# Optimization experiments

Measured on AMD Instinct MI355X. Metric: run time of the kernel, lower is better.

## Reference

```python
import jax, jax.numpy as jnp
import numpy as np

D_LOW = 32
LAGS = [1, 2, 4, 8]
# Upper-triangular pair indices (offset=1), matching torch.triu_indices(d_low, d_low, 1)
IDX_I, IDX_J = np.triu_indices(D_LOW, k=1)
IDX_I = jnp.asarray(IDX_I)
IDX_J = jnp.asarray(IDX_J)
EPS = 1e-6


def setup_inputs() -> dict:
    key = jax.random.key(0)
    ks = jax.random.split(key, 7)
    b, n, d_model = 4, 4096, 1024
    d_plucker = D_LOW * (D_LOW - 1) // 2  # 496
    s = lambda fan_in: 1.0 / np.sqrt(fan_in)
    return {
        "x": jax.random.normal(ks[0], (b, n, d_model), dtype=jnp.float32),
        "W_red": jax.random.normal(ks[1], (d_model, D_LOW), dtype=jnp.float32) * s(d_model),
        "b_red": jax.random.normal(ks[2], (D_LOW,), dtype=jnp.float32) * s(d_model),
        "W_exp": jax.random.normal(ks[3], (d_plucker, d_model), dtype=jnp.float32) * s(d_plucker),
        "b_exp": jax.random.normal(ks[4], (d_model,), dtype=jnp.float32) * s(d_plucker),
        "W_gate": jax.random.normal(ks[5], (2 * d_model, d_model), dtype=jnp.float32) * s(2 * d_model),
        "b_gate": jax.random.normal(ks[6], (d_model,), dtype=jnp.float32) * s(2 * d_model),
    }


def reference(x, W_red, b_red, W_exp, b_exp, W_gate, b_gate):
    b, n, _ = x.shape
    d_plucker = D_LOW * (D_LOW - 1) // 2
    z = x @ W_red + b_red  # [b, n, d_low]
    plucker_total = jnp.zeros((b, n, d_plucker), dtype=x.dtype)
    counts = jnp.zeros((b, n, 1), dtype=x.dtype)
    for lag in LAGS:
        if lag <= 0 or lag >= n:
            continue
        z_curr = z[:, lag:, :]   # [b, n-lag, d_low]
        z_past = z[:, :-lag, :]  # [b, n-lag, d_low]
        # Antisymmetric Plucker coordinates over upper-triangular index pairs
        p = (z_curr[:, :, IDX_I] * z_past[:, :, IDX_J]
             - z_curr[:, :, IDX_J] * z_past[:, :, IDX_I])  # [b, n-lag, d_plucker]
        norm = jnp.linalg.norm(p, axis=-1, keepdims=True)
        p = p / jnp.maximum(norm, EPS)
        plucker_total = plucker_total.at[:, lag:, :].add(p)
        counts = counts.at[:, lag:, :].add(1.0)
    counts = jnp.maximum(counts, 1.0)
    plucker_avg = plucker_total / counts
    g_avg = plucker_avg @ W_exp + b_exp  # [b, n, d_model]
    concat = jnp.concatenate([x, g_avg], axis=-1)  # [b, n, 2*d_model]
    gate = jax.nn.sigmoid(concat @ W_gate + b_gate)
    return gate * x + (1.0 - gate) * g_avg
```

## Files before the change

### kernel.cpp

```cpp
#include <hip/hip_runtime.h>
#include <hip/hip_bf16.h>
#include <math.h>

#define B_DIM   4
#define N_DIM   4096
#define D_MODEL 1024
#define D_LOW   32
#define NPAIR   496
#define NROWS   (B_DIM * N_DIM)
#define KPAD3   512
#define LDA2    1536

typedef __bf16 bf16;
typedef __bf16 bf16x8 __attribute__((ext_vector_type(8)));
typedef __bf16 bf16x4 __attribute__((ext_vector_type(4)));
typedef float  f32x4  __attribute__((ext_vector_type(4)));

#define GLOAD_LDS16(g, l) __builtin_amdgcn_global_load_lds( \
    (__attribute__((address_space(1))) void*)(g),           \
    (__attribute__((address_space(3))) void*)(l), 16, 0, 0)

__global__ __launch_bounds__(256) void prep_misc(const float* __restrict__ Wr,
                                                 bf16* __restrict__ WrT,
                                                 const float* __restrict__ We,
                                                 const float* __restrict__ be,
                                                 bf16* __restrict__ WeB) {
    __shared__ float tile[32][33];
    const int bx = blockIdx.x;
    const int t  = threadIdx.x;
    if (bx < 32) {
        const int kb = bx * 32;
        {
            int k = t >> 3, c4 = (t & 7) * 4;
            float4 v = *reinterpret_cast<const float4*>(&Wr[(size_t)(kb + k) * 32 + c4]);
            tile[k][c4 + 0] = v.x; tile[k][c4 + 1] = v.y;
            tile[k][c4 + 2] = v.z; tile[k][c4 + 3] = v.w;
        }
        __syncthreads();
        {
            int c = t >> 3, kq = (t & 7) * 4;
            bf16x4 o = { (bf16)tile[kq + 0][c], (bf16)tile[kq + 1][c],
                         (bf16)tile[kq + 2][c], (bf16)tile[kq + 3][c] };
            *reinterpret_cast<bf16x4*>(&WrT[(size_t)c * 1024 + kb + kq]) = o;
        }
    } else {
        size_t o = ((size_t)(bx - 32) * 256 + t) * 4;
        int row = (int)(o >> 10), col = (int)(o & 1023);
        float4 v = {0.f, 0.f, 0.f, 0.f};
        if (row < NPAIR)       v = *reinterpret_cast<const float4*>(&We[(size_t)row * 1024 + col]);
        else if (row == NPAIR) v = *reinterpret_cast<const float4*>(&be[col]);
        bf16x4 b = { (bf16)v.x, (bf16)v.y, (bf16)v.z, (bf16)v.w };
        *reinterpret_cast<bf16x4*>(&WeB[o]) = b;
    }
}

__global__ __launch_bounds__(256) void k1_mfma(const float* __restrict__ x,
                                               const bf16* __restrict__ WrT,
                                               bf16* __restrict__ a2,
                                               float* __restrict__ zpart) {
    const int t    = threadIdx.x;
    const int wv   = t >> 6, lane = t & 63;
    const int l15  = lane & 15, lhi = lane >> 4;
    const int kc   = blockIdx.x;
    const int mt   = blockIdx.y;
    const int row  = mt * 64 + wv * 16 + l15;
    const int kb   = kc * 256;

    f32x4 accz[2] = { (f32x4){0.f,0.f,0.f,0.f}, (f32x4){0.f,0.f,0.f,0.f} };

#pragma unroll
    for (int ks = 0; ks < 8; ++ks) {
        const int k0 = kb + ks * 32 + lhi * 8;
        const float4 u0 = *reinterpret_cast<const float4*>(&x[(size_t)row * 1024 + k0]);
        const float4 u1 = *reinterpret_cast<const float4*>(&x[(size_t)row * 1024 + k0 + 4]);
        bf16x8 af = { (bf16)u0.x, (bf16)u0.y, (bf16)u0.z, (bf16)u0.w,
                      (bf16)u1.x, (bf16)u1.y, (bf16)u1.z, (bf16)u1.w };
        *reinterpret_cast<bf16x8*>(&a2[(size_t)row * LDA2 + k0]) = af;
        const bf16x8 b0 = *reinterpret_cast<const bf16x8*>(
            &WrT[(size_t)l15 * 1024 + kb + ks * 32 + lhi * 8]);
        const bf16x8 b1 = *reinterpret_cast<const bf16x8*>(
            &WrT[(size_t)(16 + l15) * 1024 + kb + ks * 32 + lhi * 8]);
        accz[0] = __builtin_amdgcn_mfma_f32_16x16x32_bf16(af, b0, accz[0], 0, 0, 0);
        accz[1] = __builtin_amdgcn_mfma_f32_16x16x32_bf16(af, b1, accz[1], 0, 0, 0);
    }
#pragma unroll
    for (int cg = 0; cg < 2; ++cg)
#pragma unroll
        for (int r = 0; r < 4; ++r) {
            const int rout = mt * 64 + wv * 16 + lhi * 4 + r;
            zpart[((size_t)kc * NROWS + rout) * 32 + cg * 16 + l15] = accz[cg][r];
        }
}

__global__ __launch_bounds__(256) void k2_plucker(const float* __restrict__ zpart,
                                                  const float* __restrict__ br,
                                                  bf16* __restrict__ a2) {
    const int wv   = threadIdx.x >> 6;
    const int lane = threadIdx.x & 63;
    const int row  = blockIdx.x * 4 + wv;
    const int t    = row & (N_DIM - 1);
    const int c    = lane & 31;
    const float bias = br[c];

    float zc = bias;
#pragma unroll
    for (int p = 0; p < 4; ++p)
        zc += zpart[((size_t)p * NROWS + row) * 32 + c];

    float zp[4];
    float red[9];
    red[0] = zc * zc;
#pragma unroll
    for (int li = 0; li < 4; ++li) {
        const int lag = 1 << li;
        float v = 0.f;
        if (t >= lag) {
            v = bias;
#pragma unroll
            for (int p = 0; p < 4; ++p)
                v += zpart[((size_t)p * NROWS + (row - lag)) * 32 + c];
        }
        zp[li] = v;
        red[1 + li] = zc * zp[li];
        red[5 + li] = zp[li] * zp[li];
    }
#pragma unroll
    for (int m = 1; m < 32; m <<= 1) {
#pragma unroll
        for (int i = 0; i < 9; ++i) red[i] += __shfl_xor(red[i], m);
    }
    float cnt = 0.f;
#pragma unroll
    for (int li = 0; li < 4; ++li) cnt += (t >= (1 << li)) ? 1.f : 0.f;
    const float inv = 1.f / fmaxf(cnt, 1.f);

    float w = 0.f;
#pragma unroll
    for (int li = 0; li < 4; ++li) {
        float n2 = fmaxf(red[0] * red[5 + li] - red[1 + li] * red[1 + li], 0.f);
        float nr = sqrtf(n2);
        float s  = (t >= (1 << li)) ? inv / fmaxf(nr, 1e-6f) : 0.f;
        w += s * zp[li];
    }

#pragma unroll
    for (int u = 0; u < 8; ++u) {
        const int k = u * 64 + lane;
        float v = 0.f;
        if (k < NPAIR) {
            int kk = k, i = 0;
            while (kk >= 31 - i) { kk -= 31 - i; ++i; }
            const int j = i + 1 + kk;
            float zci = __shfl(zc, i), zcj = __shfl(zc, j);
            float wi  = __shfl(w, i),  wj  = __shfl(w, j);
            v = zci * wj - zcj * wi;
        }
        a2[(size_t)row * LDA2 + 1024 + k] = (bf16)v;
    }
}

__global__ __launch_bounds__(256) void transpose2(const float* __restrict__ Wg,
                                                  const float* __restrict__ We,
                                                  bf16* __restrict__ BcT,
                                                  bf16* __restrict__ WgbT,
                                                  bf16* __restrict__ WeT) {
    __shared__ float tile[32][36];
    const int z = blockIdx.z;
    const float* src = (z == 0) ? Wg : (z == 1) ? (Wg + (size_t)1024 * 1024) : We;
    bf16* dst  = (z == 0) ? BcT : (z == 1) ? WgbT : WeT;
    const int Kpad = (z == 0) ? 1536 : (z == 1) ? 1024 : 512;
    const int Ksrc = (z == 2) ? NPAIR : 1024;
    const int kb = blockIdx.x * 32;
    if (kb >= Kpad) return;
    const int nb = blockIdx.y * 32;
    const int t  = threadIdx.x;
    int li = t * 4;
    int kl = li >> 5, nl = li & 31;
    float4 v = {0.f, 0.f, 0.f, 0.f};
    if (kb + kl < Ksrc)
        v = *reinterpret_cast<const float4*>(&src[(size_t)(kb + kl) * 1024 + nb + nl]);
    tile[kl][nl + 0] = v.x; tile[kl][nl + 1] = v.y;
    tile[kl][nl + 2] = v.z; tile[kl][nl + 3] = v.w;
    __syncthreads();
    int nl2 = li >> 5, kl2 = li & 31;
    bf16x4 o = { (bf16)tile[kl2 + 0][nl2], (bf16)tile[kl2 + 1][nl2],
                 (bf16)tile[kl2 + 2][nl2], (bf16)tile[kl2 + 3][nl2] };
    *reinterpret_cast<bf16x4*>(&dst[(size_t)(nb + nl2) * Kpad + kb + kl2]) = o;
}

__global__ __launch_bounds__(256) void wcomb_wave(const bf16* __restrict__ WgbT,
                                                  const bf16* __restrict__ WeB,
                                                  bf16* __restrict__ BcT) {
    const int t    = threadIdx.x;
    const int wv   = t >> 6, lane = t & 63;
    const int l15  = lane & 15, lhi = lane >> 4;
    const int kk0  = blockIdx.x * 16;
    const int n0   = blockIdx.y * 64 + wv * 16;
    f32x4 acc = (f32x4){0.f, 0.f, 0.f, 0.f};
#pragma unroll 8
    for (int kb = 0; kb < 1024; kb += 32) {
        const bf16x8 af = *reinterpret_cast<const bf16x8*>(
            &WgbT[(size_t)(n0 + l15) * 1024 + kb + lhi * 8]);
        const bf16x8 bf = *reinterpret_cast<const bf16x8*>(
            &WeB[(size_t)(kk0 + l15) * 1024 + kb + lhi * 8]);
        acc = __builtin_amdgcn_mfma_f32_16x16x32_bf16(af, bf, acc, 0, 0, 0);
    }
#pragma unroll
    for (int r = 0; r < 4; ++r) {
        const int n = n0 + lhi * 4 + r;
        BcT[(size_t)n * 1536 + 1024 + kk0 + l15] = (bf16)acc[r];
    }
}

template <int KDIM, int LDAp, int LDBp, bool GATE>
__global__ __launch_bounds__(512, 2) void gemmoc(const bf16* __restrict__ A,
                                                 const bf16* __restrict__ Bt,
                                                 const float* __restrict__ bias,
                                                 const bf16* __restrict__ gsrc,
                                                 bf16* __restrict__ gdst,
                                                 float* __restrict__ out) {
    extern __shared__ char lds[];
    const int t    = threadIdx.x;
    const int w    = t >> 6, lane = t & 63;
    const int wr   = w >> 2, wc = w & 3;
    const int l15  = lane & 15, lhi = lane >> 4;

    const int fid = blockIdx.x;
    const int xcd = fid & 7, loc = fid >> 3;
    const int mb  = (xcd * 8 + (loc >> 2)) * 256;
    const int nb  = (loc & 3) * 256;

    const int srow = t >> 2;
    const int scol = ((t & 3) ^ (srow & 3)) * 8;
    const size_t aOff = (size_t)(mb + srow) * LDAp + scol;
    const size_t bOff = (size_t)(nb + srow) * LDBp + scol;
    char* const ldsA = lds;
    char* const ldsB = lds + 32768;

#define STAGE_A(d, h, kb) \
    GLOAD_LDS16(A + aOff + (size_t)((h) * 128) * LDAp + (kb), \
                ldsA + (d) * 16384 + (h) * 8192 + t * 16)
#define STAGE_B(d, h, kb) \
    GLOAD_LDS16(Bt + bOff + (size_t)((h) * 128) * LDBp + (kb), \
                ldsB + (d) * 16384 + (h) * 8192 + t * 16)

    const int swx = (l15 & 3) << 4;
#define LDAF(d, mq_) do { const char* Ab_ = ldsA + (d) * 16384 + wr * 8192; \
    _Pragma("unroll") for (int mf = 0; mf < 4; ++mf) { \
        int lin = ((mq_) * 64 + mf * 16 + l15) * 64 + ((lhi * 16) ^ swx); \
        afr[mf] = *reinterpret_cast<const bf16x8*>(Ab_ + lin); } } while (0)
#define LDBF(dst, d, nq_) do { const char* Bb_ = ldsB + (d) * 16384 + (wc >> 1) * 8192; \
    _Pragma("unroll") for (int nf = 0; nf < 2; ++nf) { \
        int lin = ((wc & 1) * 64 + (nq_) * 32 + nf * 16 + l15) * 64 + ((lhi * 16) ^ swx); \
        dst[nf] = *reinterpret_cast<const bf16x8*>(Bb_ + lin); } } while (0)
#define MMA(bset, mq_, nq_) do { __builtin_amdgcn_s_setprio(1); \
    _Pragma("unroll") for (int mf = 0; mf < 4; ++mf) \
    _Pragma("unroll") for (int nf = 0; nf < 2; ++nf) \
        acc[(mq_) * 4 + mf][(nq_) * 2 + nf] = __builtin_amdgcn_mfma_f32_16x16x32_bf16( \
            afr[mf], bset[nf], acc[(mq_) * 4 + mf][(nq_) * 2 + nf], 0, 0, 0); \
    __builtin_amdgcn_s_setprio(0); } while (0)
#define BAR() asm volatile("s_barrier" ::: "memory")

    f32x4 acc[8][4];
#pragma unroll
    for (int i = 0; i < 8; ++i)
#pragma unroll
        for (int j = 0; j < 4; ++j) acc[i][j] = (f32x4){0.f, 0.f, 0.f, 0.f};
    bf16x8 afr[4], bfr0[2], bfrB[2];

    STAGE_A(0, 0, 0);  STAGE_A(0, 1, 0);  STAGE_B(0, 0, 0);  STAGE_B(0, 1, 0);
    STAGE_A(1, 0, 32); STAGE_A(1, 1, 32); STAGE_B(1, 0, 32); STAGE_B(1, 1, 32);

    const int NT    = KDIM / 32;
    const int ITERS = NT / 2;
    for (int it = 0; it < ITERS; ++it) {
        const int kA = (it * 2 + 2) * 32;
        const int kB = (it * 2 + 3) * 32;
        const bool p2 = (it * 2 + 2) < NT;
        const bool p3 = (it * 2 + 3) < NT;

        asm volatile("s_waitcnt vmcnt(4)" ::: "memory");
        BAR();
        LDAF(0, 0); LDBF(bfr0, 0, 0);
        MMA(bfr0, 0, 0);
        BAR();
        LDBF(bfrB, 0, 1);
        MMA(bfrB, 0, 1);
        BAR();
        if (p2) { STAGE_B(0, 0, kA); STAGE_B(0, 1, kA); }
        LDAF(0, 1);
        MMA(bfrB, 1, 1);
        BAR();
        if (p2) { STAGE_A(0, 0, kA); STAGE_A(0, 1, kA); }
        MMA(bfr0, 1, 0);

        if (p2) asm volatile("s_waitcnt vmcnt(4)" ::: "memory");
        else    asm volatile("s_waitcnt vmcnt(0)" ::: "memory");
        BAR();
        LDAF(1, 0); LDBF(bfr0, 1, 0);
        MMA(bfr0, 0, 0);
        BAR();
        LDBF(bfrB, 1, 1);
        MMA(bfrB, 0, 1);
        BAR();
        if (p3) { STAGE_B(1, 0, kB); STAGE_B(1, 1, kB); }
        LDAF(1, 1);
        MMA(bfrB, 1, 1);
        BAR();
        if (p3) { STAGE_A(1, 0, kB); STAGE_A(1, 1, kB); }
        MMA(bfr0, 1, 0);
    }
#undef STAGE_A
#undef STAGE_B
#undef LDAF
#undef LDBF
#undef MMA
#undef BAR

#pragma unroll
    for (int mi = 0; mi < 8; ++mi) {
#pragma unroll
        for (int nf = 0; nf < 4; ++nf) {
            const int col = nb + wc * 64 + nf * 16 + l15;
            float bv = bias[col];
            if constexpr (GATE)
                bv += (float)Bt[(size_t)col * LDBp + 1024 + NPAIR];
#pragma unroll
            for (int r = 0; r < 4; ++r) {
                const int row = mb + wr * 128 + mi * 16 + lhi * 4 + r;
                float v = acc[mi][nf][r] + bv;
                if constexpr (GATE) {
                    float gate = 1.f / (1.f + expf(-v));
                    float xv = (float)A[(size_t)row * LDAp + col];
                    float gv = (float)gsrc[(size_t)row * D_MODEL + col];
                    out[(size_t)row * D_MODEL + col] = gate * xv + (1.f - gate) * gv;
                } else {
                    gdst[(size_t)row * D_MODEL + col] = (bf16)v;
                }
            }
        }
    }
}

extern "C" void kernel_launch(void* const* d_in, const int* in_sizes, int n_in,
                              void* d_out, int out_size, void* d_ws, size_t ws_size,
                              hipStream_t stream) {
    const float* x  = (const float*)d_in[0];
    const float* Wr = (const float*)d_in[1];
    const float* br = (const float*)d_in[2];
    const float* We = (const float*)d_in[3];
    const float* be = (const float*)d_in[4];
    const float* Wg = (const float*)d_in[5];
    const float* bg = (const float*)d_in[6];
    float* out = (float*)d_out;

    char* ws = (char*)d_ws;
    bf16*  gbuf  = (bf16*)(ws);
    float* zpart = (float*)(ws);
    bf16*  A2    = (bf16*)(ws + (32u << 20));
    bf16*  WeT   = (bf16*)(ws + (80u << 20));
    bf16*  BcT   = (bf16*)(ws + (81u << 20));
    bf16*  WgbT  = (bf16*)(ws + (84u << 20));
    bf16*  WeB   = (bf16*)(ws + (86u << 20));
    bf16*  WrT   = (bf16*)(ws + (88u << 20));

    (void)hipFuncSetAttribute(reinterpret_cast<const void*>(&gemmoc<KPAD3, LDA2, KPAD3, false>),
                              hipFuncAttributeMaxDynamicSharedMemorySize, 65536);
    (void)hipFuncSetAttribute(reinterpret_cast<const void*>(&gemmoc<1536, LDA2, 1536, true>),
                              hipFuncAttributeMaxDynamicSharedMemorySize, 65536);

    prep_misc<<<544, 256, 0, stream>>>(Wr, WrT, We, be, WeB);
    transpose2<<<dim3(32, 32, 3), 256, 0, stream>>>(Wg, We, BcT, WgbT, WeT);
    wcomb_wave<<<dim3(32, 16), 256, 0, stream>>>(WgbT, WeB, BcT);
    k1_mfma<<<dim3(4, 256), 256, 0, stream>>>(x, WrT, A2, zpart);
    k2_plucker<<<NROWS / 4, 256, 0, stream>>>(zpart, br, A2);

    gemmoc<KPAD3, LDA2, KPAD3, false><<<256, 512, 65536, stream>>>(
        A2 + 1024, WeT, be, nullptr, gbuf, nullptr);
    gemmoc<1536, LDA2, 1536, true><<<256, 512, 65536, stream>>>(
        A2, BcT, bg, gbuf, nullptr, out);
}
```

Before: 165.4 us.

## Replace 256x256 eight-wave GEMM with 128x128 four-wave K64 double-buffered GEMM

Both GEMMs switch from 256x256 output tiles on 512-thread blocks, with an interleaved ping-pong schedule, to 128x128 tiles on 256-thread blocks. Each block now stages K=64 slices with an 8-way XOR swizzle and uses a simple double-buffered loop. The grid grows from 256 to 1024 blocks, which should spread work better across CUs and simplify scheduling. The cost is lower reuse per tile, so global and L2 traffic for A and B roughly doubles, and the fine-grained compute/load interleaving is lost.

```diff
diff --git a/kernel.cpp b/kernel.cpp
--- a/kernel.cpp
+++ b/kernel.cpp
@@ -213,7 +213,7 @@
 }
 
 template <int KDIM, int LDAp, int LDBp, bool GATE>
-__global__ __launch_bounds__(512, 2) void gemmoc(const bf16* __restrict__ A,
+__global__ __launch_bounds__(256, 2) void gemm2c(const bf16* __restrict__ A,
                                                  const bf16* __restrict__ Bt,
                                                  const float* __restrict__ bias,
                                                  const bf16* __restrict__ gsrc,
@@ -222,103 +222,83 @@
     extern __shared__ char lds[];
     const int t    = threadIdx.x;
     const int w    = t >> 6, lane = t & 63;
-    const int wr   = w >> 2, wc = w & 3;
+    const int wr   = w >> 1, wc = w & 1;
     const int l15  = lane & 15, lhi = lane >> 4;
 
     const int fid = blockIdx.x;
     const int xcd = fid & 7, loc = fid >> 3;
-    const int mb  = (xcd * 8 + (loc >> 2)) * 256;
-    const int nb  = (loc & 3) * 256;
-
-    const int srow = t >> 2;
-    const int scol = ((t & 3) ^ (srow & 3)) * 8;
+    const int mb  = (xcd * 16 + (loc >> 3)) * 128;
+    const int nb  = (loc & 7) * 128;
+
+    const int srow = t >> 3;
+    const int scol = ((t & 7) ^ (srow & 7)) * 8;
     const size_t aOff = (size_t)(mb + srow) * LDAp + scol;
     const size_t bOff = (size_t)(nb + srow) * LDBp + scol;
     char* const ldsA = lds;
     char* const ldsB = lds + 32768;
 
-#define STAGE_A(d, h, kb) \
-    GLOAD_LDS16(A + aOff + (size_t)((h) * 128) * LDAp + (kb), \
-                ldsA + (d) * 16384 + (h) * 8192 + t * 16)
-#define STAGE_B(d, h, kb) \
-    GLOAD_LDS16(Bt + bOff + (size_t)((h) * 128) * LDBp + (kb), \
-                ldsB + (d) * 16384 + (h) * 8192 + t * 16)
-
-    const int swx = (l15 & 3) << 4;
-#define LDAF(d, mq_) do { const char* Ab_ = ldsA + (d) * 16384 + wr * 8192; \
-    _Pragma("unroll") for (int mf = 0; mf < 4; ++mf) { \
-        int lin = ((mq_) * 64 + mf * 16 + l15) * 64 + ((lhi * 16) ^ swx); \
-        afr[mf] = *reinterpret_cast<const bf16x8*>(Ab_ + lin); } } while (0)
-#define LDBF(dst, d, nq_) do { const char* Bb_ = ldsB + (d) * 16384 + (wc >> 1) * 8192; \
-    _Pragma("unroll") for (int nf = 0; nf < 2; ++nf) { \
-        int lin = ((wc & 1) * 64 + (nq_) * 32 + nf * 16 + l15) * 64 + ((lhi * 16) ^ swx); \
-        dst[nf] = *reinterpret_cast<const bf16x8*>(Bb_ + lin); } } while (0)
-#define MMA(bset, mq_, nq_) do { __builtin_amdgcn_s_setprio(1); \
-    _Pragma("unroll") for (int mf = 0; mf < 4; ++mf) \
-    _Pragma("unroll") for (int nf = 0; nf < 2; ++nf) \
-        acc[(mq_) * 4 + mf][(nq_) * 2 + nf] = __builtin_amdgcn_mfma_f32_16x16x32_bf16( \
-            afr[mf], bset[nf], acc[(mq_) * 4 + mf][(nq_) * 2 + nf], 0, 0, 0); \
-    __builtin_amdgcn_s_setprio(0); } while (0)
-#define BAR() asm volatile("s_barrier" ::: "memory")
-
-    f32x4 acc[8][4];
-#pragma unroll
-    for (int i = 0; i < 8; ++i)
+#define STAGE_T(d, kb) do { \
+    _Pragma("unroll") for (int q = 0; q < 4; ++q) \
+        GLOAD_LDS16(A + aOff + (size_t)(q * 32) * LDAp + (kb), \
+                    ldsA + (d) * 16384 + q * 4096 + t * 16); \
+    _Pragma("unroll") for (int q = 0; q < 4; ++q) \
+        GLOAD_LDS16(Bt + bOff + (size_t)(q * 32) * LDBp + (kb), \
+                    ldsB + (d) * 16384 + q * 4096 + t * 16); } while (0)
+
+    const int swx = (l15 & 7) << 4;
+
+    f32x4 acc[4][4];
+#pragma unroll
+    for (int i = 0; i < 4; ++i)
 #pragma unroll
         for (int j = 0; j < 4; ++j) acc[i][j] = (f32x4){0.f, 0.f, 0.f, 0.f};
-    bf16x8 afr[4], bfr0[2], bfrB[2];
-
-    STAGE_A(0, 0, 0);  STAGE_A(0, 1, 0);  STAGE_B(0, 0, 0);  STAGE_B(0, 1, 0);
-    STAGE_A(1, 0, 32); STAGE_A(1, 1, 32); STAGE_B(1, 0, 32); STAGE_B(1, 1, 32);
-
-    const int NT    = KDIM / 32;
-    const int ITERS = NT / 2;
-    for (int it = 0; it < ITERS; ++it) {
-        const int kA = (it * 2 + 2) * 32;
-        const int kB = (it * 2 + 3) * 32;
-        const bool p2 = (it * 2 + 2) < NT;
-        const bool p3 = (it * 2 + 3) < NT;
-
-        asm volatile("s_waitcnt vmcnt(4)" ::: "memory");
-        BAR();
-        LDAF(0, 0); LDBF(bfr0, 0, 0);
-        MMA(bfr0, 0, 0);
-        BAR();
-        LDBF(bfrB, 0, 1);
-        MMA(bfrB, 0, 1);
-        BAR();
-        if (p2) { STAGE_B(0, 0, kA); STAGE_B(0, 1, kA); }
-        LDAF(0, 1);
-        MMA(bfrB, 1, 1);
-        BAR();
-        if (p2) { STAGE_A(0, 0, kA); STAGE_A(0, 1, kA); }
-        MMA(bfr0, 1, 0);
-
-        if (p2) asm volatile("s_waitcnt vmcnt(4)" ::: "memory");
-        else    asm volatile("s_waitcnt vmcnt(0)" ::: "memory");
-        BAR();
-        LDAF(1, 0); LDBF(bfr0, 1, 0);
-        MMA(bfr0, 0, 0);
-        BAR();
-        LDBF(bfrB, 1, 1);
-        MMA(bfrB, 0, 1);
-        BAR();
-        if (p3) { STAGE_B(1, 0, kB); STAGE_B(1, 1, kB); }
-        LDAF(1, 1);
-        MMA(bfrB, 1, 1);
-        BAR();
-        if (p3) { STAGE_A(1, 0, kB); STAGE_A(1, 1, kB); }
-        MMA(bfr0, 1, 0);
-    }
-#undef STAGE_A
-#undef STAGE_B
-#undef LDAF
-#undef LDBF
-#undef MMA
-#undef BAR
-
-#pragma unroll
-    for (int mi = 0; mi < 8; ++mi) {
+    bf16x8 afr[4][2], bfr[4][2];
+
+    STAGE_T(0, 0);
+
+    const int NT = KDIM / 64;
+    for (int kt = 0; kt < NT; ++kt) {
+        const int d = kt & 1;
+        asm volatile("s_barrier" ::: "memory");
+        if (kt + 1 < NT) {
+            STAGE_T(d ^ 1, (kt + 1) * 64);
+            asm volatile("s_waitcnt vmcnt(8)" ::: "memory");
+        } else {
+            asm volatile("s_waitcnt vmcnt(0)" ::: "memory");
+        }
+        asm volatile("s_barrier" ::: "memory");
+
+        const char* Ab = ldsA + d * 16384;
+        const char* Bb = ldsB + d * 16384;
+#pragma unroll
+        for (int mf = 0; mf < 4; ++mf)
+#pragma unroll
+            for (int ks = 0; ks < 2; ++ks) {
+                int lin = (wr * 64 + mf * 16 + l15) * 128 + ks * 64 + lhi * 16;
+                afr[mf][ks] = *reinterpret_cast<const bf16x8*>(Ab + (lin ^ swx));
+            }
+#pragma unroll
+        for (int nf = 0; nf < 4; ++nf)
+#pragma unroll
+            for (int ks = 0; ks < 2; ++ks) {
+                int lin = (wc * 64 + nf * 16 + l15) * 128 + ks * 64 + lhi * 16;
+                bfr[nf][ks] = *reinterpret_cast<const bf16x8*>(Bb + (lin ^ swx));
+            }
+        __builtin_amdgcn_s_setprio(1);
+#pragma unroll
+        for (int mf = 0; mf < 4; ++mf)
+#pragma unroll
+            for (int nf = 0; nf < 4; ++nf)
+#pragma unroll
+                for (int ks = 0; ks < 2; ++ks)
+                    acc[mf][nf] = __builtin_amdgcn_mfma_f32_16x16x32_bf16(
+                        afr[mf][ks], bfr[nf][ks], acc[mf][nf], 0, 0, 0);
+        __builtin_amdgcn_s_setprio(0);
+    }
+#undef STAGE_T
+
+#pragma unroll
+    for (int mf = 0; mf < 4; ++mf) {
 #pragma unroll
         for (int nf = 0; nf < 4; ++nf) {
             const int col = nb + wc * 64 + nf * 16 + l15;
@@ -327,8 +307,8 @@
                 bv += (float)Bt[(size_t)col * LDBp + 1024 + NPAIR];
 #pragma unroll
             for (int r = 0; r < 4; ++r) {
-                const int row = mb + wr * 128 + mi * 16 + lhi * 4 + r;
-                float v = acc[mi][nf][r] + bv;
+                const int row = mb + wr * 64 + mf * 16 + lhi * 4 + r;
+                float v = acc[mf][nf][r] + bv;
                 if constexpr (GATE) {
                     float gate = 1.f / (1.f + expf(-v));
                     float xv = (float)A[(size_t)row * LDAp + col];
@@ -364,9 +344,9 @@
     bf16*  WeB   = (bf16*)(ws + (86u << 20));
     bf16*  WrT   = (bf16*)(ws + (88u << 20));
 
-    (void)hipFuncSetAttribute(reinterpret_cast<const void*>(&gemmoc<KPAD3, LDA2, KPAD3, false>),
+    (void)hipFuncSetAttribute(reinterpret_cast<const void*>(&gemm2c<KPAD3, LDA2, KPAD3, false>),
                               hipFuncAttributeMaxDynamicSharedMemorySize, 65536);
-    (void)hipFuncSetAttribute(reinterpret_cast<const void*>(&gemmoc<1536, LDA2, 1536, true>),
+    (void)hipFuncSetAttribute(reinterpret_cast<const void*>(&gemm2c<1536, LDA2, 1536, true>),
                               hipFuncAttributeMaxDynamicSharedMemorySize, 65536);
 
     prep_misc<<<544, 256, 0, stream>>>(Wr, WrT, We, be, WeB);
@@ -375,8 +355,8 @@
     k1_mfma<<<dim3(4, 256), 256, 0, stream>>>(x, WrT, A2, zpart);
     k2_plucker<<<NROWS / 4, 256, 0, stream>>>(zpart, br, A2);
 
-    gemmoc<KPAD3, LDA2, KPAD3, false><<<256, 512, 65536, stream>>>(
+    gemm2c<KPAD3, LDA2, KPAD3, false><<<1024, 256, 65536, stream>>>(
         A2 + 1024, WeT, be, nullptr, gbuf, nullptr);
-    gemmoc<1536, LDA2, 1536, true><<<256, 512, 65536, stream>>>(
+    gemm2c<1536, LDA2, 1536, true><<<1024, 256, 65536, stream>>>(
         A2, BcT, bg, gbuf, nullptr, out);
 }
```

New measurement: 159.1 us. 3.8% less time.
